# Optimization experiments

Hardware: AMD Instinct MI355X
Metric: run time of the kernel (lower is better)

Reference implementation:

```python
import jax, jax.numpy as jnp
import numpy as np

SIGMA = 1.0   # kernel influence distance (init kwarg)
RADIUS = 1.0  # kernel radius (kernel points live within this ball)


def setup_inputs() -> dict:
    key = jax.random.key(0)
    k0, k1, k2, k3, k4, k5 = jax.random.split(key, 6)
    N, M, H, K, Cin, Cout = 50000, 50000, 32, 15, 64, 64
    q_points = jax.random.normal(k0, (M, 3), dtype=jnp.float32)
    s_points = jax.random.normal(k1, (N, 3), dtype=jnp.float32)
    s_feats = jax.random.normal(k2, (N, Cin), dtype=jnp.float32)
    # index == N selects the padded 'fantom' point (zero features, far away)
    neighbor_indices = jax.random.randint(k3, (M, H), 0, N + 1, dtype=jnp.int64)
    kernel_points = jax.random.normal(k4, (K, 3), dtype=jnp.float32) * (0.4 * RADIUS)
    weights = jax.random.normal(k5, (K, Cin, Cout), dtype=jnp.float32) * 0.05
    return {
        'q_points': q_points,
        's_points': s_points,
        's_feats': s_feats,
        'neighbor_indices': neighbor_indices,
        'kernel_points': kernel_points,
        'weights': weights,
    }


def reference(q_points, s_points, s_feats, neighbor_indices, kernel_points, weights):
    # Pad source points with a far-away fantom point and zero features so that
    # neighbor_indices == N behaves as an empty neighbor slot.
    s_pts = jnp.concatenate([s_points, jnp.full((1, 3), 1e6, s_points.dtype)], axis=0)
    s_fts = jnp.concatenate([s_feats, jnp.zeros((1, s_feats.shape[1]), s_feats.dtype)], axis=0)

    # Gather neighbors and center on query points: (M, H, 3)
    neighbors = s_pts[neighbor_indices] - q_points[:, None, :]
    # Distances to each kernel point: (M, H, K)
    diffs = neighbors[:, :, None, :] - kernel_points[None, None, :, :]
    sq_dists = jnp.sum(diffs * diffs, axis=-1)
    # Linear kernel influence (KPConv 'linear' mode): (M, H, K)
    influence = jnp.maximum(1.0 - jnp.sqrt(sq_dists) / SIGMA, 0.0)
    # Fantom neighbors are ~1e6 away -> influence exactly 0.

    # Gather neighbor features: (M, H, Cin)
    nb_feats = s_fts[neighbor_indices]
    # Weight features by kernel influence, reduce over neighbors: (M, K, Cin)
    weighted = jnp.einsum('mhk,mhc->mkc', influence, nb_feats)
    # Apply per-kernel-point linear maps and sum over kernel points: (M, Cout)
    out = jnp.einsum('mkc,kcd->md', weighted, weights)

    # Normalize by the number of valid (non-zero-feature) neighbors.
    feat_sum = jnp.sum(nb_feats, axis=-1)               # (M, H)
    nnum = jnp.maximum(jnp.sum(feat_sum > 0.0, axis=-1), 1)  # (M,)
    return out / nnum[:, None].astype(out.dtype)
```

## Files before the change

### kernel.cpp

```cpp
#include <hip/hip_runtime.h>

#define NPTS 50000
#define MPTS 50000
#define HN 32
#define KCD 960
#define PSTRIDE 968
#define FSTRIDE 40

typedef float f32x4 __attribute__((ext_vector_type(4)));
typedef short s16x8 __attribute__((ext_vector_type(8)));

__device__ __forceinline__ unsigned short bf_rne(float x) {
    union { float f; unsigned u; } v; v.f = x;
    unsigned r = v.u + 0x7fffu + ((v.u >> 16) & 1u);
    return (unsigned short)(r >> 16);
}
__device__ __forceinline__ unsigned short bf_trunc(float x) {
    union { float f; unsigned u; } v; v.f = x;
    return (unsigned short)(v.u >> 16);
}

__global__ __launch_bounds__(256) void prep(const float* __restrict__ w,
                                            const float* __restrict__ feats,
                                            unsigned short* __restrict__ WT,
                                            unsigned char* __restrict__ signs) {
    int b = blockIdx.x;
    if (b < 240) {
        int t = b * 256 + threadIdx.x;
        int kc = t >> 6, d = t & 63;
        WT[d * KCD + kc] = bf_rne(w[t]);
    } else {
        int lane = threadIdx.x & 63, wv = threadIdx.x >> 6;
        int r4 = lane >> 4, c16 = lane & 15;
        int n = (b - 240) * 16 + wv * 4 + r4;
        float4 v = *(const float4*)(feats + (size_t)n * 64 + c16 * 4);
        float s = v.x + v.y + v.z + v.w;
        s += __shfl_xor(s, 1); s += __shfl_xor(s, 2);
        s += __shfl_xor(s, 4); s += __shfl_xor(s, 8);
        if (c16 == 0) signs[n] = (s > 0.f) ? 1 : 0;
    }
}

__global__ __launch_bounds__(256, 3)
void kpconv_main(const float* __restrict__ q_points,
                 const float* __restrict__ s_points,
                 const float* __restrict__ s_feats,
                 const int* __restrict__ ni,
                 const float* __restrict__ kpts,
                 const unsigned short* __restrict__ WT,
                 const unsigned char* __restrict__ signs,
                 float* __restrict__ out) {
    __shared__ __align__(16) unsigned short P_sh[16][PSTRIDE];
    __shared__ __align__(16) unsigned short feats_sh[4][64][FSTRIDE];
    __shared__ __align__(16) float rpos_sh[4][3][32];
    __shared__ float kp_sh[16][3];
    __shared__ float q_sh[16][3];
    __shared__ float inv_nnum[16];

    int tid = threadIdx.x, w = tid >> 6, lane = tid & 63;
    int m_base = blockIdx.x << 4;

    if (tid < 48) {
        kp_sh[tid / 3][tid % 3] = (tid < 45) ? kpts[tid] : 1e9f;
        q_sh[tid / 3][tid % 3] = q_points[m_base * 3 + tid];
    }
    __syncthreads();

    int h = lane & 31;
    int row = lane & 15, quad = lane >> 4, kq = quad << 3;
    int h2 = lane >> 1, half = lane & 1;

    float kx = kp_sh[row][0], ky = kp_sh[row][1], kz = kp_sh[row][2];

    float tkx[8], tky[8], tkz[8];
    #pragma unroll
    for (int j = 0; j < 8; ++j) {
        int k = half * 8 + j;
        tkx[j] = kp_sh[k][0]; tky[j] = kp_sh[k][1]; tkz[j] = kp_sh[k][2];
    }

    int idx4[4]; float rxa[4], rya[4], rza[4]; unsigned char sg4[4];
    #pragma unroll
    for (int mi = 0; mi < 4; ++mi)
        idx4[mi] = ni[(m_base + mi * 4 + w) * HN + h];
    #pragma unroll
    for (int mi = 0; mi < 4; ++mi) {
        int m_l = mi * 4 + w;
        bool valid = idx4[mi] < NPTS;
        const float* sp = s_points + (size_t)(valid ? idx4[mi] : 0) * 3;
        float px = sp[0], py = sp[1], pz = sp[2];
        unsigned char sg = signs[valid ? idx4[mi] : 0];
        rxa[mi] = (valid ? px : 1e6f) - q_sh[m_l][0];
        rya[mi] = (valid ? py : 1e6f) - q_sh[m_l][1];
        rza[mi] = (valid ? pz : 1e6f) - q_sh[m_l][2];
        sg4[mi] = valid ? sg : 0;
    }

    bool alive2[4]; int idx2c[4];
    #pragma unroll
    for (int mi = 0; mi < 4; ++mi) {
        float rx2 = __shfl(rxa[mi], h2);
        float ry2 = __shfl(rya[mi], h2);
        float rz2 = __shfl(rza[mi], h2);
        int idx2 = __shfl(idx4[mi], h2);
        int av = 0;
        #pragma unroll
        for (int j = 0; j < 8; ++j) {
            float dx = rx2 - tkx[j], dy = ry2 - tky[j], dz = rz2 - tkz[j];
            float d2 = dx * dx + dy * dy + dz * dz;
            av |= (d2 < 1.f) ? 1 : 0;
        }
        av |= __shfl_xor(av, 1);
        alive2[mi] = (idx2 < NPTS) && (av != 0);
        idx2c[mi] = idx2 < NPTS ? idx2 : 0;
    }

    float4 fv[2][8];
    #define ISSUE(buf, mi)                                                        \
        {                                                                         \
            _Pragma("unroll")                                                     \
            for (int j = 0; j < 8; ++j) fv[buf][j] = float4{0.f, 0.f, 0.f, 0.f};  \
            if (alive2[mi]) {                                                     \
                const float4* fp =                                                \
                    (const float4*)(s_feats + (size_t)idx2c[mi] * 64 + half * 32);\
                _Pragma("unroll")                                                 \
                for (int j = 0; j < 8; ++j) {                                     \
                    int jj = (j + half) & 7;                                      \
                    fv[buf][j] = fp[jj];                                          \
                }                                                                 \
            }                                                                     \
        }

    ISSUE(0, 0)

    #pragma unroll
    for (int mi = 0; mi < 4; ++mi) {
        int cur = mi & 1;
        if (mi < 3) { ISSUE(1 - cur, mi + 1) }

        int m_l = mi * 4 + w;
        if (lane < 32) {
            rpos_sh[w][0][h] = rxa[mi];
            rpos_sh[w][1][h] = rya[mi];
            rpos_sh[w][2][h] = rza[mi];
        }

        unsigned long long pm = __ballot((lane < 32) && (idx4[mi] < NPTS) && sg4[mi]);
        if (lane == 0) {
            int cnt = __popcll(pm);
            inv_nnum[m_l] = 1.f / (float)(cnt < 1 ? 1 : cnt);
        }

        float4 ra0 = *(const float4*)&rpos_sh[w][0][kq];
        float4 ra1 = *(const float4*)&rpos_sh[w][0][kq + 4];
        float4 rb0 = *(const float4*)&rpos_sh[w][1][kq];
        float4 rb1 = *(const float4*)&rpos_sh[w][1][kq + 4];
        float4 rc0 = *(const float4*)&rpos_sh[w][2][kq];
        float4 rc1 = *(const float4*)&rpos_sh[w][2][kq + 4];
        float hx[8] = {ra0.x, ra0.y, ra0.z, ra0.w, ra1.x, ra1.y, ra1.z, ra1.w};
        float hy[8] = {rb0.x, rb0.y, rb0.z, rb0.w, rb1.x, rb1.y, rb1.z, rb1.w};
        float hz[8] = {rc0.x, rc0.y, rc0.z, rc0.w, rc1.x, rc1.y, rc1.z, rc1.w};
        s16x8 afrag;
        #pragma unroll
        for (int j = 0; j < 8; ++j) {
            float dx = hx[j] - kx, dy = hy[j] - ky, dz = hz[j] - kz;
            float d2 = dx * dx + dy * dy + dz * dz;
            float infl = 1.f - sqrtf(d2);
            infl = infl > 0.f ? infl : 0.f;
            afrag[j] = (short)bf_trunc(infl);
        }

        #pragma unroll
        for (int j = 0; j < 8; ++j) {
            int jj = (j + half) & 7;
            int c = half * 32 + jj * 4;
            float4 v = fv[cur][j];
            feats_sh[w][c + 0][h2] = bf_trunc(v.x);
            feats_sh[w][c + 1][h2] = bf_trunc(v.y);
            feats_sh[w][c + 2][h2] = bf_trunc(v.z);
            feats_sh[w][c + 3][h2] = bf_trunc(v.w);
        }

        #pragma unroll
        for (int ch = 0; ch < 4; ++ch) {
            s16x8 bfrag = *(const s16x8*)&feats_sh[w][ch * 16 + row][kq];
            f32x4 acc = {0.f, 0.f, 0.f, 0.f};
            acc = __builtin_amdgcn_mfma_f32_16x16x32_bf16(afrag, bfrag, acc, 0, 0, 0);
            int cc = ch * 16 + row;
            #pragma unroll
            for (int r = 0; r < 4; ++r) {
                int k2 = quad * 4 + r;
                if (k2 < 15) {
                    int col = (k2 << 6) | (cc ^ ((k2 >> 2) << 4));
                    P_sh[m_l][col] = bf_trunc(acc[r]);
                }
            }
        }
    }
    __syncthreads();

    {
        int dbase = w << 4;
        f32x4 acc = {0.f, 0.f, 0.f, 0.f};
        const unsigned short* wtp = WT + (size_t)(dbase + row) * KCD + kq;
        #pragma unroll 6
        for (int s = 0; s < 30; ++s) {
            int k = s >> 1;
            int c0 = ((s & 1) << 5) + kq;
            int cx = c0 ^ (((k >> 2) & 3) << 4);
            s16x8 a = *(const s16x8*)&P_sh[row][(k << 6) | cx];
            s16x8 b = *(const s16x8*)&wtp[s * 32];
            acc = __builtin_amdgcn_mfma_f32_16x16x32_bf16(a, b, acc, 0, 0, 0);
        }
        #pragma unroll
        for (int r = 0; r < 4; ++r) {
            int m_l = quad * 4 + r;
            out[(size_t)(m_base + m_l) * 64 + dbase + row] = acc[r] * inv_nnum[m_l];
        }
    }
}

extern "C" void kernel_launch(void* const* d_in, const int* in_sizes, int n_in,
                              void* d_out, int out_size, void* d_ws, size_t ws_size,
                              hipStream_t stream) {
    const float* q  = (const float*)d_in[0];
    const float* sp = (const float*)d_in[1];
    const float* sf = (const float*)d_in[2];
    const int*   ni = (const int*)d_in[3];
    const float* kp = (const float*)d_in[4];
    const float* wt = (const float*)d_in[5];
    float* out = (float*)d_out;

    unsigned short* WT = (unsigned short*)d_ws;
    unsigned char* signs = (unsigned char*)d_ws + 64 * KCD * 2;

    hipLaunchKernelGGL(prep, dim3(240 + NPTS / 16), dim3(256), 0, stream,
                       wt, sf, WT, signs);
    hipLaunchKernelGGL(kpconv_main, dim3(MPTS / 16), dim3(256), 0, stream,
                       q, sp, sf, ni, kp, WT, signs, out);
}
```

Before: 164.2 us.

## Gather neighbor features directly into MFMA B-fragments, drop feature LDS staging

Neighbor features are no longer loaded as coalesced float4 rows into registers and transposed through a shared-memory tile. Instead, the surviving neighbor indices go to a small LDS table, and each lane gathers scalar floats straight into its MFMA B-fragment layout, packing bf16 pairs with a byte-permute. This removes the LDS transpose and its write/read traffic and cuts shared memory enough to raise the occupancy target from 3 to 4 blocks. The cost is many uncoalesced 4-byte global loads in place of 16-byte vector loads, and the loss of the double-buffered prefetch that overlapped gathers with compute.

```diff
diff --git a/kernel.cpp b/kernel.cpp
--- a/kernel.cpp
+++ b/kernel.cpp
@@ -5,7 +5,6 @@
 #define HN 32
 #define KCD 960
 #define PSTRIDE 968
-#define FSTRIDE 40
 
 typedef float f32x4 __attribute__((ext_vector_type(4)));
 typedef short s16x8 __attribute__((ext_vector_type(8)));
@@ -18,6 +17,10 @@
 __device__ __forceinline__ unsigned short bf_trunc(float x) {
     union { float f; unsigned u; } v; v.f = x;
     return (unsigned short)(v.u >> 16);
+}
+__device__ __forceinline__ unsigned pack_bf(float lo, float hi) {
+    union { float f; unsigned u; } a, b; a.f = lo; b.f = hi;
+    return __builtin_amdgcn_perm(b.u, a.u, 0x07060302u);
 }
 
 __global__ __launch_bounds__(256) void prep(const float* __restrict__ w,
@@ -41,7 +44,7 @@
     }
 }
 
-__global__ __launch_bounds__(256, 3)
+__global__ __launch_bounds__(256, 4)
 void kpconv_main(const float* __restrict__ q_points,
                  const float* __restrict__ s_points,
                  const float* __restrict__ s_feats,
@@ -51,8 +54,8 @@
                  const unsigned char* __restrict__ signs,
                  float* __restrict__ out) {
     __shared__ __align__(16) unsigned short P_sh[16][PSTRIDE];
-    __shared__ __align__(16) unsigned short feats_sh[4][64][FSTRIDE];
     __shared__ __align__(16) float rpos_sh[4][3][32];
+    __shared__ int ni_sh[4][4][32];
     __shared__ float kp_sh[16][3];
     __shared__ float q_sh[16][3];
     __shared__ float inv_nnum[16];
@@ -96,7 +99,6 @@
         sg4[mi] = valid ? sg : 0;
     }
 
-    bool alive2[4]; int idx2c[4];
     #pragma unroll
     for (int mi = 0; mi < 4; ++mi) {
         float rx2 = __shfl(rxa[mi], h2);
@@ -111,33 +113,18 @@
             av |= (d2 < 1.f) ? 1 : 0;
         }
         av |= __shfl_xor(av, 1);
-        alive2[mi] = (idx2 < NPTS) && (av != 0);
-        idx2c[mi] = idx2 < NPTS ? idx2 : 0;
-    }
-
-    float4 fv[2][8];
-    #define ISSUE(buf, mi)                                                        \
-        {                                                                         \
-            _Pragma("unroll")                                                     \
-            for (int j = 0; j < 8; ++j) fv[buf][j] = float4{0.f, 0.f, 0.f, 0.f};  \
-            if (alive2[mi]) {                                                     \
-                const float4* fp =                                                \
-                    (const float4*)(s_feats + (size_t)idx2c[mi] * 64 + half * 32);\
-                _Pragma("unroll")                                                 \
-                for (int j = 0; j < 8; ++j) {                                     \
-                    int jj = (j + half) & 7;                                      \
-                    fv[buf][j] = fp[jj];                                          \
-                }                                                                 \
-            }                                                                     \
-        }
-
-    ISSUE(0, 0)
+        bool alive = (idx2 < NPTS) && (av != 0);
+        if (half == 0) ni_sh[w][mi][h2] = alive ? idx2 : NPTS;
+
+        unsigned long long pm = __ballot((lane < 32) && (idx4[mi] < NPTS) && sg4[mi]);
+        if (lane == 0) {
+            int cnt = __popcll(pm);
+            inv_nnum[mi * 4 + w] = 1.f / (float)(cnt < 1 ? 1 : cnt);
+        }
+    }
 
     #pragma unroll
     for (int mi = 0; mi < 4; ++mi) {
-        int cur = mi & 1;
-        if (mi < 3) { ISSUE(1 - cur, mi + 1) }
-
         int m_l = mi * 4 + w;
         if (lane < 32) {
             rpos_sh[w][0][h] = rxa[mi];
@@ -145,10 +132,15 @@
             rpos_sh[w][2][h] = rza[mi];
         }
 
-        unsigned long long pm = __ballot((lane < 32) && (idx4[mi] < NPTS) && sg4[mi]);
-        if (lane == 0) {
-            int cnt = __popcll(pm);
-            inv_nnum[m_l] = 1.f / (float)(cnt < 1 ? 1 : cnt);
+        float g0[8], g1[8], g2[8], g3[8];
+        #pragma unroll
+        for (int j = 0; j < 8; ++j) {
+            int idxj = ni_sh[w][mi][kq + j];
+            g0[j] = 0.f; g1[j] = 0.f; g2[j] = 0.f; g3[j] = 0.f;
+            if (idxj < NPTS) {
+                const float* fp = s_feats + (size_t)idxj * 64 + row;
+                g0[j] = fp[0]; g1[j] = fp[16]; g2[j] = fp[32]; g3[j] = fp[48];
+            }
         }
 
         float4 ra0 = *(const float4*)&rpos_sh[w][0][kq];
@@ -160,32 +152,26 @@
         float hx[8] = {ra0.x, ra0.y, ra0.z, ra0.w, ra1.x, ra1.y, ra1.z, ra1.w};
         float hy[8] = {rb0.x, rb0.y, rb0.z, rb0.w, rb1.x, rb1.y, rb1.z, rb1.w};
         float hz[8] = {rc0.x, rc0.y, rc0.z, rc0.w, rc1.x, rc1.y, rc1.z, rc1.w};
-        s16x8 afrag;
+        float infl[8];
         #pragma unroll
         for (int j = 0; j < 8; ++j) {
             float dx = hx[j] - kx, dy = hy[j] - ky, dz = hz[j] - kz;
             float d2 = dx * dx + dy * dy + dz * dz;
-            float infl = 1.f - sqrtf(d2);
-            infl = infl > 0.f ? infl : 0.f;
-            afrag[j] = (short)bf_trunc(infl);
-        }
-
-        #pragma unroll
-        for (int j = 0; j < 8; ++j) {
-            int jj = (j + half) & 7;
-            int c = half * 32 + jj * 4;
-            float4 v = fv[cur][j];
-            feats_sh[w][c + 0][h2] = bf_trunc(v.x);
-            feats_sh[w][c + 1][h2] = bf_trunc(v.y);
-            feats_sh[w][c + 2][h2] = bf_trunc(v.z);
-            feats_sh[w][c + 3][h2] = bf_trunc(v.w);
-        }
+            float f = 1.f - sqrtf(d2);
+            infl[j] = f > 0.f ? f : 0.f;
+        }
+        union { unsigned u[4]; s16x8 v; } af;
+        #pragma unroll
+        for (int p = 0; p < 4; ++p) af.u[p] = pack_bf(infl[2 * p], infl[2 * p + 1]);
 
         #pragma unroll
         for (int ch = 0; ch < 4; ++ch) {
-            s16x8 bfrag = *(const s16x8*)&feats_sh[w][ch * 16 + row][kq];
+            const float* gs = (ch == 0) ? g0 : (ch == 1) ? g1 : (ch == 2) ? g2 : g3;
+            union { unsigned u[4]; s16x8 v; } bf;
+            #pragma unroll
+            for (int p = 0; p < 4; ++p) bf.u[p] = pack_bf(gs[2 * p], gs[2 * p + 1]);
             f32x4 acc = {0.f, 0.f, 0.f, 0.f};
-            acc = __builtin_amdgcn_mfma_f32_16x16x32_bf16(afrag, bfrag, acc, 0, 0, 0);
+            acc = __builtin_amdgcn_mfma_f32_16x16x32_bf16(af.v, bf.v, acc, 0, 0, 0);
             int cc = ch * 16 + row;
             #pragma unroll
             for (int r = 0; r < 4; ++r) {
```

Result: faster. 152.9 us (-6.8%).
